# Performance work log

Measured on AMD Instinct MI355X. Metric: run time of the kernel, lower is better.

## Reference

```python
import jax, jax.numpy as jnp
import numpy as np
import math

D_MODEL = 1024
RANK = 128
K_RANK = 128
N_KNOW = 32768
COARSE_K = 64
FINE_K = 16
B, S = 2, 2048


def setup_inputs() -> dict:
    key = jax.random.key(0)
    ks = jax.random.split(key, 6)
    x = jax.random.normal(ks[0], (B, S, D_MODEL), dtype=jnp.float32)
    h = jax.random.normal(ks[1], (B, S, RANK), dtype=jnp.float32)
    W_router = jax.random.normal(ks[2], (D_MODEL, N_KNOW), dtype=jnp.float32) * 0.02
    W_q = jax.random.normal(ks[3], (K_RANK, RANK), dtype=jnp.float32) * 0.02  # Linear(rank->k_rank) weight
    K_all = jax.random.normal(ks[4], (N_KNOW, K_RANK), dtype=jnp.float32) * 0.02
    V_all = jax.random.normal(ks[5], (N_KNOW, D_MODEL), dtype=jnp.float32) * 0.02
    return {"x": x, "h": h, "W_router": W_router, "W_q": W_q, "K_all": K_all, "V_all": V_all}


def reference(x, h, W_router, W_q, K_all, V_all):
    # Stage 1: coarse candidate selection via router logits
    k_logits = jnp.einsum('bsd,dn->bsn', x, W_router)              # [B,S,N]
    coarse_scores, candidate_idx = jax.lax.top_k(k_logits, COARSE_K)  # [B,S,Ck]

    # Stage 2: fine matching with compressed query
    query = jnp.einsum('bsr,kr->bsk', h, W_q)                      # [B,S,K_RANK]
    K_cand = K_all[candidate_idx]                                  # [B,S,Ck,K_RANK] gather
    fine_scores = jnp.einsum('bsd,bscd->bsc', query, K_cand) / math.sqrt(K_RANK)
    fine_topk_scores, fine_local_idx = jax.lax.top_k(fine_scores, FINE_K)  # [B,S,Fk]
    fine_weights = jax.nn.softmax(fine_topk_scores, axis=-1)
    fine_global_idx = jnp.take_along_axis(candidate_idx, fine_local_idx, axis=-1)  # [B,S,Fk]

    selected_V = V_all[fine_global_idx]                            # [B,S,Fk,D] gather
    output = jnp.einsum('bsfd,bsf->bsd', selected_V, fine_weights)  # weighted combine
    return output
```

## Files before the change

kernel.cpp:

```cpp
#include <hip/hip_runtime.h>
#include <cstdint>

#define D_MODEL 1024
#define RANK 128
#define K_RANK_ 128
#define N_KNOW 32768
#define COARSE_K 64
#define FINE_K 16
#define NTOK 4096
#define MSEL 96
#define DELTA 1.15e-3f
#define SC 4096
#define QSCALE 8192.0f
#define QINV (1.0f / 8192.0f)

using u32 = unsigned int;
using u64 = unsigned long long;
typedef _Float16 half8 __attribute__((ext_vector_type(8)));
typedef __attribute__((ext_vector_type(4))) float f32x4;

__device__ __forceinline__ u32 ordf(float v) {
    u32 u = __float_as_uint(v);
    return (u & 0x80000000u) ? ~u : (u | 0x80000000u);
}
__device__ __forceinline__ ushort f2h(float f) {
    union { _Float16 h; ushort u; } cv; cv.h = (_Float16)f; return cv.u;
}
__device__ __forceinline__ void gload16(const void* g, void* l) {
    __builtin_amdgcn_global_load_lds(
        (const __attribute__((address_space(1))) char*)g,
        (__attribute__((address_space(3))) char*)l, 16, 0, 0);
}

__global__ __launch_bounds__(256)
void kcvt_x(const float* __restrict__ in, ushort* __restrict__ xh)
{
    int i = blockIdx.x * 256 + threadIdx.x;
    float4 v = ((const float4*)in)[i];
    ((ushort4*)xh)[i] = make_ushort4(f2h(v.x), f2h(v.y), f2h(v.z), f2h(v.w));
}

__global__ __launch_bounds__(256)
void kcvt_wt(const float* __restrict__ W, ushort* __restrict__ out, int col0)
{
    __shared__ float tile[32][33];
    const int nb = blockIdx.x * 32;
    const int kb = blockIdx.y * 32;
    const int tx = threadIdx.x & 31, ty = threadIdx.x >> 5;
#pragma unroll
    for (int q = 0; q < 4; ++q)
        tile[ty + q * 8][tx] = W[(size_t)(kb + ty + q * 8) * N_KNOW + col0 + nb + tx];
    __syncthreads();
#pragma unroll
    for (int q = 0; q < 4; ++q) {
        float v = tile[tx][ty + q * 8];
        out[(size_t)(nb + ty + q * 8) * D_MODEL + kb + tx] = f2h(v);
    }
}

__global__ __launch_bounds__(512, 2)
void k1f8(const ushort* __restrict__ xh, const ushort* __restrict__ wt,
          ushort* __restrict__ L)
{
    __shared__ ushort lds[2][32768];

    const int tid = threadIdx.x;
    const int nwg = gridDim.x;
    int wfl = blockIdx.x;
    wfl = (wfl & 7) * (nwg >> 3) + (wfl >> 3);
    const int bm = (wfl & 15) * 256;
    const int bn = (wfl >> 4) * 256;

    const int lane = tid & 63;
    const int wid = tid >> 6;
    const int wm = wid >> 2, wn = wid & 3;
    const int lr = lane & 15, g = lane >> 4;

    const ushort* gA[4]; const ushort* gB[4];
#pragma unroll
    for (int i = 0; i < 4; ++i) {
        const int o = i * 512 + tid;
        const int row = o >> 3;
        const int gslot = (o & 7) ^ (row & 7);
        gA[i] = xh + (size_t)(bm + row) * D_MODEL + gslot * 8;
        gB[i] = wt + (size_t)(bn + row) * D_MODEL + gslot * 8;
    }

    int aoff[2][8], boff[2][4];
#pragma unroll
    for (int ks = 0; ks < 2; ++ks) {
#pragma unroll
        for (int mf = 0; mf < 8; ++mf) {
            int row = wm * 128 + mf * 16 + lr;
            aoff[ks][mf] = row * 128 + (((ks * 4 + g) ^ (row & 7)) << 4);
        }
#pragma unroll
        for (int nf = 0; nf < 4; ++nf) {
            int row = wn * 64 + nf * 16 + lr;
            boff[ks][nf] = 32768 + row * 128 + (((ks * 4 + g) ^ (row & 7)) << 4);
        }
    }

    f32x4 acc[8][4];
#pragma unroll
    for (int mf = 0; mf < 8; ++mf)
#pragma unroll
        for (int nf = 0; nf < 4; ++nf) acc[mf][nf] = (f32x4)(0.f);

#define SAH(b, t, h)                                                           \
    {                                                                          \
        gload16(gA[2*(h)]   + (t) * 64,                                        \
                (char*)&lds[(b)][0] + ((2*(h)) * 512 + tid) * 16);             \
        gload16(gA[2*(h)+1] + (t) * 64,                                        \
                (char*)&lds[(b)][0] + ((2*(h)+1) * 512 + tid) * 16);           \
    }
#define SBH(b, t, h)                                                           \
    {                                                                          \
        gload16(gB[2*(h)]   + (t) * 64,                                        \
                (char*)&lds[(b)][0] + 32768 + ((2*(h)) * 512 + tid) * 16);     \
        gload16(gB[2*(h)+1] + (t) * 64,                                        \
                (char*)&lds[(b)][0] + 32768 + ((2*(h)+1) * 512 + tid) * 16);   \
    }

#define LDA4(lb, ks, base)                                                     \
    a0 = *(const half8*)((lb) + aoff[ks][(base) + 0]);                         \
    a1 = *(const half8*)((lb) + aoff[ks][(base) + 1]);                         \
    a2 = *(const half8*)((lb) + aoff[ks][(base) + 2]);                         \
    a3 = *(const half8*)((lb) + aoff[ks][(base) + 3]);

#define LDB4(lb, ks, bb)                                                       \
    bb[0] = *(const half8*)((lb) + boff[ks][0]);                               \
    bb[1] = *(const half8*)((lb) + boff[ks][1]);                               \
    bb[2] = *(const half8*)((lb) + boff[ks][2]);                               \
    bb[3] = *(const half8*)((lb) + boff[ks][3]);

#define MFMA16(mbase, bb)                                                      \
    __builtin_amdgcn_s_setprio(1);                                             \
    _Pragma("unroll")                                                          \
    for (int nf = 0; nf < 4; ++nf) {                                           \
        acc[(mbase)+0][nf] = __builtin_amdgcn_mfma_f32_16x16x32_f16(           \
            a0, bb[nf], acc[(mbase)+0][nf], 0, 0, 0);                          \
        acc[(mbase)+1][nf] = __builtin_amdgcn_mfma_f32_16x16x32_f16(           \
            a1, bb[nf], acc[(mbase)+1][nf], 0, 0, 0);                          \
        acc[(mbase)+2][nf] = __builtin_amdgcn_mfma_f32_16x16x32_f16(           \
            a2, bb[nf], acc[(mbase)+2][nf], 0, 0, 0);                          \
        acc[(mbase)+3][nf] = __builtin_amdgcn_mfma_f32_16x16x32_f16(           \
            a3, bb[nf], acc[(mbase)+3][nf], 0, 0, 0);                          \
    }                                                                          \
    __builtin_amdgcn_s_setprio(0);

#define SBAR()                                                                 \
    __builtin_amdgcn_sched_barrier(0);                                         \
    __builtin_amdgcn_s_barrier();                                              \
    __builtin_amdgcn_sched_barrier(0);

    SBH(0, 0, 0); SBH(0, 0, 1);
    SAH(0, 0, 0); SAH(0, 0, 1);
    SBH(1, 1, 0); SBH(1, 1, 1);

    const char* lb0 = (const char*)&lds[0][0];
    const char* lb1 = (const char*)&lds[1][0];
    half8 b0q[4], b1q[4];

    for (int i = 0; i < 8; ++i) {
        const int t1 = 2 * i + 1;
        const int tn0 = 2 * i + 2, tn1 = 2 * i + 3;
        const bool st = tn0 < 16;
        half8 a0, a1, a2, a3;

        asm volatile("s_waitcnt vmcnt(4)" ::: "memory");
        SBAR();
        LDA4(lb0, 0, 0);
        LDB4(lb0, 0, b0q);
        SAH(1, t1, 0);
        MFMA16(0, b0q);
        LDA4(lb0, 1, 0);
        LDB4(lb0, 1, b1q);
        SAH(1, t1, 1);
        MFMA16(0, b1q);
        SBAR();
        LDA4(lb0, 0, 4);
        if (st) SBH(0, tn0, 0);
        MFMA16(4, b0q);
        LDA4(lb0, 1, 4);
        if (st) SBH(0, tn0, 1);
        MFMA16(4, b1q);
        if (i < 7) asm volatile("s_waitcnt vmcnt(4)" ::: "memory");
        else       asm volatile("s_waitcnt vmcnt(0)" ::: "memory");
        SBAR();
        LDA4(lb1, 0, 0);
        LDB4(lb1, 0, b0q);
        if (st) SAH(0, tn0, 0);
        MFMA16(0, b0q);
        LDA4(lb1, 1, 0);
        LDB4(lb1, 1, b1q);
        if (st) SAH(0, tn0, 1);
        MFMA16(0, b1q);
        SBAR();
        LDA4(lb1, 0, 4);
        if (st) SBH(1, tn1, 0);
        MFMA16(4, b0q);
        LDA4(lb1, 1, 4);
        if (st) SBH(1, tn1, 1);
        MFMA16(4, b1q);
    }
#undef SAH
#undef SBH
#undef LDA4
#undef LDB4
#undef MFMA16
#undef SBAR

    const int crow0 = bm + wm * 128 + g * 4;
    const int ccol  = bn + wn * 64 + lr;
#pragma unroll
    for (int mf = 0; mf < 8; ++mf)
#pragma unroll
        for (int nf = 0; nf < 4; ++nf)
#pragma unroll
            for (int r = 0; r < 4; ++r) {
                int q = __float2int_rn(acc[mf][nf][r] * QSCALE) + 32768;
                q = q < 0 ? 0 : (q > 65535 ? 65535 : q);
                L[(size_t)(crow0 + mf * 16 + r) * SC + ccol + nf * 16] = (ushort)q;
            }
}

template <int M>
__global__ __launch_bounds__(256)
void k2_topk(const ushort* __restrict__ L, u64* __restrict__ R,
             int col0, int stripe)
{
    const int tt = blockIdx.x;
    const int tid = threadIdx.x;

    __shared__ u64 buf[4224];
    __shared__ int scnt;
    __shared__ int sred[4];

    u64 key[16];
    const uint4* row8 = (const uint4*)(L + (size_t)tt * SC);
#pragma unroll
    for (int q = 0; q < 2; ++q) {
        uint4 v = row8[q * 256 + tid];
        const int c = col0 + (q * 256 + tid) * 8;
        u32 wv[4] = {v.x, v.y, v.z, v.w};
#pragma unroll
        for (int d = 0; d < 4; ++d) {
            key[q * 8 + d * 2]     = ((u64)(wv[d] & 0xFFFFu) << 32) | (u32)(N_KNOW - 1 - (c + d * 2));
            key[q * 8 + d * 2 + 1] = ((u64)(wv[d] >> 16) << 32)    | (u32)(N_KNOW - 2 - (c + d * 2));
        }
    }

    u64 tkey;
    if (stripe == 0) {
        u32 lo = 0, hi = 65536;
        for (int it = 0; it < 17; ++it) {
            if (hi - lo <= 1) break;
            u32 mid = lo + ((hi - lo) >> 1);
            int c = 0;
#pragma unroll
            for (int j = 0; j < 16; ++j) c += ((u32)(key[j] >> 32) > mid) ? 1 : 0;
#pragma unroll
            for (int o = 32; o; o >>= 1) c += __shfl_xor(c, o);
            if ((tid & 63) == 0) sred[tid >> 6] = c;
            __syncthreads();
            c = sred[0] + sred[1] + sred[2] + sred[3];
            __syncthreads();
            if (c >= M) { lo = mid; if (c <= 768) break; }
            else hi = mid;
        }
        tkey = ((u64)lo << 32) | 0xFFFFFFFFull;
        if (tid == 0) scnt = 0;
    } else {
        tkey = R[(size_t)tt * M + (M - 1)];
        if (tid < M) buf[tid] = R[(size_t)tt * M + tid];
        if (tid == 0) scnt = M;
    }
    __syncthreads();

#pragma unroll
    for (int j = 0; j < 16; ++j)
        if (key[j] > tkey) {
            int p = atomicAdd(&scnt, 1);
            if (p < 4224) buf[p] = key[j];
        }
    __syncthreads();

    const int n = min(scnt, 4224);
    for (int i = tid; i < n; i += 256) {
        u64 ki = buf[i];
        int r = 0;
        for (int j = 0; j < n; ++j) r += (buf[j] > ki) ? 1 : 0;
        if (r < M) R[(size_t)tt * M + r] = ki;
    }
}

__global__ __launch_bounds__(256)
void k2b_band(const u64* __restrict__ R96, u32* __restrict__ jobs,
              int* __restrict__ jobCount, u32* __restrict__ band)
{
    __shared__ float sv[4][MSEL];
    const int tid = threadIdx.x;
    const int w = tid >> 6, lane = tid & 63;
    const int tt = blockIdx.x * 4 + w;

    sv[w][lane] = ((int)(u32)(R96[(size_t)tt * MSEL + lane] >> 32) - 32768) * QINV;
    if (lane < MSEL - 64)
        sv[w][lane + 64] = ((int)(u32)(R96[(size_t)tt * MSEL + lane + 64] >> 32) - 32768) * QINV;
    __syncthreads();

    const float t = sv[w][COARSE_K - 1];
    int cg = 0, cl = 0;
    for (int j = lane; j < MSEL; j += 64) {
        cg += (sv[w][j] > t + DELTA) ? 1 : 0;
        cl += (sv[w][j] < t - DELTA) ? 1 : 0;
    }
#pragma unroll
    for (int o = 32; o; o >>= 1) { cg += __shfl_xor(cg, o); cl += __shfl_xor(cl, o); }

    int lo = cg, hi = MSEL - 1 - cl;
    if (lo > COARSE_K - 1) lo = COARSE_K - 1;
    if (hi < COARSE_K - 1) hi = COARSE_K - 1;

    u32 b;
    if (lo == COARSE_K - 1 && hi == COARSE_K - 1) {
        b = 0x80000000u | 63u | (63u << 8);
    } else {
        int nj = hi - lo + 1;
        int base = 0;
        if (lane == 0) base = atomicAdd(jobCount, nj);
        base = __shfl(base, 0);
        for (int k = lane; k < nj; k += 64)
            jobs[base + k] = ((u32)tt << 8) | (u32)(lo + k);
        b = (u32)lo | ((u32)hi << 8);
    }
    if (lane == 0) band[tt] = b;
}

__global__ __launch_bounds__(256)
void k2b_exec(const u32* __restrict__ jobs, const int* __restrict__ jobCount,
              const u64* __restrict__ R96, const float* __restrict__ x,
              const float* __restrict__ W, u64* __restrict__ nk)
{
    __shared__ float red[4];
    const int tid = threadIdx.x;
    const int n = *jobCount;
    for (int j = blockIdx.x; j < n; j += gridDim.x) {
        u32 jd = jobs[j];
        int tt = jd >> 8, idx = jd & 255;
        u64 key = R96[(size_t)tt * MSEL + idx];
        int col = (N_KNOW - 1) - (int)(u32)(key & 0xFFFFFFFFu);
        float p = 0.f;
#pragma unroll
        for (int q = 0; q < 4; ++q) {
            int k = tid + q * 256;
            p = fmaf(x[(size_t)tt * D_MODEL + k], W[(size_t)k * N_KNOW + col], p);
        }
#pragma unroll
        for (int o = 32; o; o >>= 1) p += __shfl_xor(p, o);
        if ((tid & 63) == 0) red[tid >> 6] = p;
        __syncthreads();
        if (tid == 0) {
            float e = red[0] + red[1] + red[2] + red[3];
            nk[(size_t)tt * MSEL + idx] = ((u64)ordf(e) << 32) | (key & 0xFFFFFFFFu);
        }
        __syncthreads();
    }
}

__global__ __launch_bounds__(128)
void k2b_final(const u64* __restrict__ R96, const u64* __restrict__ nk,
               const u32* __restrict__ band, u64* __restrict__ R64)
{
    const int tt = blockIdx.x;
    const int tid = threadIdx.x;
    __shared__ u64 keys[MSEL];
    __shared__ u64 nkk[MSEL];

    const u32 b = band[tt];
    if (tid < MSEL) keys[tid] = R96[(size_t)tt * MSEL + tid];
    const int lo = b & 0xFF, hi = (b >> 8) & 0xFF;
    const bool trivial = (b & 0x80000000u) != 0;
    if (!trivial && tid >= lo && tid <= hi && tid < MSEL)
        nkk[tid] = nk[(size_t)tt * MSEL + tid];
    __syncthreads();

    if (trivial) {
        if (tid < COARSE_K) R64[(size_t)tt * COARSE_K + tid] = keys[tid];
        return;
    }
    if (tid < lo) R64[(size_t)tt * COARSE_K + tid] = keys[tid];
    const int mwin = COARSE_K - lo;
    if (tid >= lo && tid <= hi) {
        u64 me = nkk[tid];
        int r = 0;
        for (int j = lo; j <= hi; ++j) r += (nkk[j] > me) ? 1 : 0;
        if (r < mwin) R64[(size_t)tt * COARSE_K + lo + r] = keys[tid];
    }
}

__device__ __forceinline__ void fma4(float4& a, float w, const float4& v) {
    a.x = fmaf(w, v.x, a.x); a.y = fmaf(w, v.y, a.y);
    a.z = fmaf(w, v.z, a.z); a.w = fmaf(w, v.w, a.w);
}

__global__ __launch_bounds__(256)
void k3f(const float* __restrict__ h, const float* __restrict__ Wq,
         const float* __restrict__ Kall, const u64* __restrict__ R,
         int* __restrict__ fidx, float* __restrict__ fw)
{
    __shared__ float hq[4][RANK];
    __shared__ float qv[4][K_RANK_];

    const int tid = threadIdx.x;
    const int w = tid >> 6, lane = tid & 63;
    const int tt = blockIdx.x * 4 + w;

    {
        float2 hv = *(const float2*)(h + (size_t)tt * RANK + lane * 2);
        hq[w][lane * 2] = hv.x;
        hq[w][lane * 2 + 1] = hv.y;
    }
    const u64 key = R[(size_t)tt * COARSE_K + lane];
    const int ci = (N_KNOW - 1) - (int)(u32)(key & 0xFFFFFFFFu);
    __syncthreads();

    {
        float s0 = 0.f, s1 = 0.f;
        const float4* w0 = (const float4*)(Wq + (size_t)(lane * 2) * RANK);
        const float4* w1 = (const float4*)(Wq + (size_t)(lane * 2 + 1) * RANK);
#pragma unroll
        for (int r4 = 0; r4 < RANK / 4; ++r4) {
            float4 a = w0[r4], b = w1[r4];
            const float* hh = &hq[w][r4 * 4];
            s0 = fmaf(a.x, hh[0], s0); s0 = fmaf(a.y, hh[1], s0);
            s0 = fmaf(a.z, hh[2], s0); s0 = fmaf(a.w, hh[3], s0);
            s1 = fmaf(b.x, hh[0], s1); s1 = fmaf(b.y, hh[1], s1);
            s1 = fmaf(b.z, hh[2], s1); s1 = fmaf(b.w, hh[3], s1);
        }
        qv[w][lane * 2] = s0;
        qv[w][lane * 2 + 1] = s1;
    }
    __syncthreads();

    float sc;
    {
        float s = 0.f;
        const float4* kr = (const float4*)(Kall + (size_t)ci * K_RANK_);
#pragma unroll
        for (int r4 = 0; r4 < K_RANK_ / 4; ++r4) {
            float4 a = kr[r4];
            const float* qq = &qv[w][r4 * 4];
            s = fmaf(a.x, qq[0], s); s = fmaf(a.y, qq[1], s);
            s = fmaf(a.z, qq[2], s); s = fmaf(a.w, qq[3], s);
        }
        sc = s * 0.08838834764831845f;
    }

    const u64 myk = ((u64)ordf(sc) << 32) | (u32)(63 - lane);
    int rnk = 0;
#pragma unroll
    for (int j = 0; j < 64; ++j) {
        u64 kj = __shfl(myk, j);
        rnk += (kj > myk) ? 1 : 0;
    }

    float smax = sc;
#pragma unroll
    for (int o = 32; o; o >>= 1) smax = fmaxf(smax, __shfl_xor(smax, o));
    float e = (rnk < FINE_K) ? expf(sc - smax) : 0.f;
    float esum = e;
#pragma unroll
    for (int o = 32; o; o >>= 1) esum += __shfl_xor(esum, o);
    if (rnk < FINE_K) {
        fidx[(size_t)tt * FINE_K + rnk] = ci;
        fw[(size_t)tt * FINE_K + rnk] = e / esum;
    }
}

__global__ __launch_bounds__(256)
void k3g(const int* __restrict__ fidx, const float* __restrict__ fw,
         const float* __restrict__ Vall, float* __restrict__ out)
{
    __shared__ int si[FINE_K];
    __shared__ float sw[FINE_K];
    const int tt = blockIdx.x;
    const int tid = threadIdx.x;
    if (tid < FINE_K) {
        si[tid] = fidx[(size_t)tt * FINE_K + tid];
        sw[tid] = fw[(size_t)tt * FINE_K + tid];
    }
    __syncthreads();

    float4 a = make_float4(0.f, 0.f, 0.f, 0.f);
#pragma unroll
    for (int f = 0; f < FINE_K; ++f) {
        const float4 v = *(const float4*)(Vall + (size_t)si[f] * D_MODEL + tid * 4);
        fma4(a, sw[f], v);
    }
    ((float4*)(out + (size_t)tt * D_MODEL))[tid] = a;
}

extern "C" void kernel_launch(void* const* d_in, const int* in_sizes, int n_in,
                              void* d_out, int out_size, void* d_ws, size_t ws_size,
                              hipStream_t stream)
{
    const float* x  = (const float*)d_in[0];
    const float* h  = (const float*)d_in[1];
    const float* Wr = (const float*)d_in[2];
    const float* Wq = (const float*)d_in[3];
    const float* Ka = (const float*)d_in[4];
    const float* Va = (const float*)d_in[5];
    float* out = (float*)d_out;

    const size_t fixed =
        (size_t)NTOK * D_MODEL * 2 +
        (size_t)NTOK * SC * 2 +
        (size_t)NTOK * MSEL * 8 * 2 +
        (size_t)NTOK * COARSE_K * 8 +
        (size_t)NTOK * MSEL * 4 +
        4096 +
        (size_t)NTOK * 4 +
        (size_t)NTOK * FINE_K * 8;

    int WCH = N_KNOW;
    while (WCH > SC && fixed + (size_t)WCH * D_MODEL * 2 > ws_size)
        WCH >>= 1;

    char* p = (char*)d_ws;
    ushort* wt   = (ushort*)p;  p += (size_t)WCH * D_MODEL * 2;
    ushort* xh   = (ushort*)p;  p += (size_t)NTOK * D_MODEL * 2;
    ushort* Lq   = (ushort*)p;  p += (size_t)NTOK * SC * 2;
    u64*    R96  = (u64*)p;     p += (size_t)NTOK * MSEL * 8;
    u64*    nk   = (u64*)p;     p += (size_t)NTOK * MSEL * 8;
    u64*    R64  = (u64*)p;     p += (size_t)NTOK * COARSE_K * 8;
    u32*    jobs = (u32*)p;     p += (size_t)NTOK * MSEL * 4;
    int*    jobCount = (int*)p; p += 4096;
    u32*    band = (u32*)p;     p += (size_t)NTOK * 4;
    int*    fidx = (int*)p;     p += (size_t)NTOK * FINE_K * 4;
    float*  fw   = (float*)p;   p += (size_t)NTOK * FINE_K * 4;

    hipMemsetAsync(jobCount, 0, 4, stream);

    kcvt_x<<<NTOK * D_MODEL / 4 / 256, 256, 0, stream>>>(x, xh);

    const int nstripe = N_KNOW / SC;
    const int spc = WCH / SC;
    for (int s = 0; s < nstripe; ++s) {
        if (s % spc == 0)
            kcvt_wt<<<dim3(WCH / 32, D_MODEL / 32), 256, 0, stream>>>(Wr, wt, s * SC);
        const ushort* wts = wt + (size_t)((s % spc) * SC) * D_MODEL;
        k1f8<<<(SC / 256) * (NTOK / 256), 512, 0, stream>>>(xh, wts, Lq);
        k2_topk<MSEL><<<NTOK, 256, 0, stream>>>(Lq, R96, s * SC, s);
    }

    k2b_band<<<NTOK / 4, 256, 0, stream>>>(R96, jobs, jobCount, band);
    k2b_exec<<<8192, 256, 0, stream>>>(jobs, jobCount, R96, x, Wr, nk);
    k2b_final<<<NTOK, 128, 0, stream>>>(R96, nk, band, R64);

    k3f<<<NTOK / 4, 256, 0, stream>>>(h, Wq, Ka, R64, fidx, fw);
    k3g<<<NTOK, 256, 0, stream>>>(fidx, fw, Va, out);
}
```

Before: 764.0 us.

## Use split-fp16 transposed router weights for contiguous band rescoring

When the workspace is large enough, the router weight is converted once into transposed fp16 hi and lo halves. The rescoring kernel then reads contiguous hi+lo rows per candidate column instead of strided fp32 column reads of W_router. This targets the uncoalesced gather cost in k2b_exec. In exchange the conversion kernel writes an extra 64MB, and hi+lo is slightly less precise than fp32.

Result: faster. 689.3 us (-9.8%).

```diff
diff --git a/kernel.cpp b/kernel.cpp
--- a/kernel.cpp
+++ b/kernel.cpp
@@ -26,6 +26,9 @@
 __device__ __forceinline__ ushort f2h(float f) {
     union { _Float16 h; ushort u; } cv; cv.h = (_Float16)f; return cv.u;
 }
+__device__ __forceinline__ float h2f(ushort u) {
+    union { ushort u; _Float16 h; } cv; cv.u = u; return (float)cv.h;
+}
 __device__ __forceinline__ void gload16(const void* g, void* l) {
     __builtin_amdgcn_global_load_lds(
         (const __attribute__((address_space(1))) char*)g,
@@ -55,6 +58,29 @@
     for (int q = 0; q < 4; ++q) {
         float v = tile[tx][ty + q * 8];
         out[(size_t)(nb + ty + q * 8) * D_MODEL + kb + tx] = f2h(v);
+    }
+}
+
+__global__ __launch_bounds__(256)
+void kcvt_wt2(const float* __restrict__ W, ushort* __restrict__ hi,
+              ushort* __restrict__ lo)
+{
+    __shared__ float tile[32][33];
+    const int nb = blockIdx.x * 32;
+    const int kb = blockIdx.y * 32;
+    const int tx = threadIdx.x & 31, ty = threadIdx.x >> 5;
+#pragma unroll
+    for (int q = 0; q < 4; ++q)
+        tile[ty + q * 8][tx] = W[(size_t)(kb + ty + q * 8) * N_KNOW + nb + tx];
+    __syncthreads();
+#pragma unroll
+    for (int q = 0; q < 4; ++q) {
+        float v = tile[tx][ty + q * 8];
+        ushort hh = f2h(v);
+        ushort ll = f2h(v - h2f(hh));
+        size_t o = (size_t)(nb + ty + q * 8) * D_MODEL + kb + tx;
+        hi[o] = hh;
+        lo[o] = ll;
     }
 }
 
@@ -368,6 +394,40 @@
     }
 }
 
+__global__ __launch_bounds__(256)
+void k2b_exec_c(const u32* __restrict__ jobs, const int* __restrict__ jobCount,
+                const u64* __restrict__ R96, const float* __restrict__ x,
+                const ushort* __restrict__ whi, const ushort* __restrict__ wlo,
+                u64* __restrict__ nk)
+{
+    __shared__ float red[4];
+    const int tid = threadIdx.x;
+    const int n = *jobCount;
+    for (int j = blockIdx.x; j < n; j += gridDim.x) {
+        u32 jd = jobs[j];
+        int tt = jd >> 8, idx = jd & 255;
+        u64 key = R96[(size_t)tt * MSEL + idx];
+        int col = (N_KNOW - 1) - (int)(u32)(key & 0xFFFFFFFFu);
+        float4 xv = ((const float4*)(x + (size_t)tt * D_MODEL))[tid];
+        ushort4 hv = ((const ushort4*)(whi + (size_t)col * D_MODEL))[tid];
+        ushort4 lv = ((const ushort4*)(wlo + (size_t)col * D_MODEL))[tid];
+        float p = 0.f;
+        p = fmaf(xv.x, h2f(hv.x) + h2f(lv.x), p);
+        p = fmaf(xv.y, h2f(hv.y) + h2f(lv.y), p);
+        p = fmaf(xv.z, h2f(hv.z) + h2f(lv.z), p);
+        p = fmaf(xv.w, h2f(hv.w) + h2f(lv.w), p);
+#pragma unroll
+        for (int o = 32; o; o >>= 1) p += __shfl_xor(p, o);
+        if ((tid & 63) == 0) red[tid >> 6] = p;
+        __syncthreads();
+        if (tid == 0) {
+            float e = red[0] + red[1] + red[2] + red[3];
+            nk[(size_t)tt * MSEL + idx] = ((u64)ordf(e) << 32) | (key & 0xFFFFFFFFu);
+        }
+        __syncthreads();
+    }
+}
+
 __global__ __launch_bounds__(128)
 void k2b_final(const u64* __restrict__ R96, const u64* __restrict__ nk,
                const u32* __restrict__ band, u64* __restrict__ R64)
@@ -523,12 +583,23 @@
         (size_t)NTOK * 4 +
         (size_t)NTOK * FINE_K * 8;
 
-    int WCH = N_KNOW;
-    while (WCH > SC && fixed + (size_t)WCH * D_MODEL * 2 > ws_size)
-        WCH >>= 1;
+    const size_t WFULL = (size_t)N_KNOW * D_MODEL * 2;
+    const bool pathA = fixed + 2 * WFULL <= ws_size;
 
     char* p = (char*)d_ws;
-    ushort* wt   = (ushort*)p;  p += (size_t)WCH * D_MODEL * 2;
+    ushort* wt   = (ushort*)p;
+    ushort* wlo  = nullptr;
+    int WCH;
+    if (pathA) {
+        WCH = N_KNOW;
+        p += WFULL;
+        wlo = (ushort*)p; p += WFULL;
+    } else {
+        WCH = N_KNOW;
+        while (WCH > SC && fixed + (size_t)WCH * D_MODEL * 2 > ws_size)
+            WCH >>= 1;
+        p += (size_t)WCH * D_MODEL * 2;
+    }
     ushort* xh   = (ushort*)p;  p += (size_t)NTOK * D_MODEL * 2;
     ushort* Lq   = (ushort*)p;  p += (size_t)NTOK * SC * 2;
     u64*    R96  = (u64*)p;     p += (size_t)NTOK * MSEL * 8;
@@ -545,17 +616,29 @@
     kcvt_x<<<NTOK * D_MODEL / 4 / 256, 256, 0, stream>>>(x, xh);
 
     const int nstripe = N_KNOW / SC;
-    const int spc = WCH / SC;
-    for (int s = 0; s < nstripe; ++s) {
-        if (s % spc == 0)
-            kcvt_wt<<<dim3(WCH / 32, D_MODEL / 32), 256, 0, stream>>>(Wr, wt, s * SC);
-        const ushort* wts = wt + (size_t)((s % spc) * SC) * D_MODEL;
-        k1f8<<<(SC / 256) * (NTOK / 256), 512, 0, stream>>>(xh, wts, Lq);
-        k2_topk<MSEL><<<NTOK, 256, 0, stream>>>(Lq, R96, s * SC, s);
+    if (pathA) {
+        kcvt_wt2<<<dim3(N_KNOW / 32, D_MODEL / 32), 256, 0, stream>>>(Wr, wt, wlo);
+        for (int s = 0; s < nstripe; ++s) {
+            const ushort* wts = wt + (size_t)(s * SC) * D_MODEL;
+            k1f8<<<(SC / 256) * (NTOK / 256), 512, 0, stream>>>(xh, wts, Lq);
+            k2_topk<MSEL><<<NTOK, 256, 0, stream>>>(Lq, R96, s * SC, s);
+        }
+    } else {
+        const int spc = WCH / SC;
+        for (int s = 0; s < nstripe; ++s) {
+            if (s % spc == 0)
+                kcvt_wt<<<dim3(WCH / 32, D_MODEL / 32), 256, 0, stream>>>(Wr, wt, s * SC);
+            const ushort* wts = wt + (size_t)((s % spc) * SC) * D_MODEL;
+            k1f8<<<(SC / 256) * (NTOK / 256), 512, 0, stream>>>(xh, wts, Lq);
+            k2_topk<MSEL><<<NTOK, 256, 0, stream>>>(Lq, R96, s * SC, s);
+        }
     }
 
     k2b_band<<<NTOK / 4, 256, 0, stream>>>(R96, jobs, jobCount, band);
-    k2b_exec<<<8192, 256, 0, stream>>>(jobs, jobCount, R96, x, Wr, nk);
+    if (pathA)
+        k2b_exec_c<<<8192, 256, 0, stream>>>(jobs, jobCount, R96, x, wt, wlo, nk);
+    else
+        k2b_exec<<<8192, 256, 0, stream>>>(jobs, jobCount, R96, x, Wr, nk);
     k2b_final<<<NTOK, 128, 0, stream>>>(R96, nk, band, R64);
 
     k3f<<<NTOK / 4, 256, 0, stream>>>(h, Wq, Ka, R64, fidx, fw);
```

## Convert router weights once into hi/lo fp16 split and select top-k over full logit rows

Applied to the files above, without the earlier changes.

Transposes W_router a single time into fp16 hi and lo halves with a wider, vectorized transpose kernel. The exact rescoring pass now reads contiguous hi+lo rows instead of strided fp32 columns. When workspace allows, the logit GEMM runs once over all 32768 columns and a new single-pass per-token selection kernel replaces the eight stripe launches. This trades a much larger workspace and a 128 MB logit buffer round trip for fewer launches and coalesced rescoring. The hi+lo sum is slightly less exact than the original fp32 weights.

Result: slower. 1.891 ms (+147.5%).

```diff
diff --git a/kernel.cpp b/kernel.cpp
--- a/kernel.cpp
+++ b/kernel.cpp
@@ -26,6 +26,9 @@
 __device__ __forceinline__ ushort f2h(float f) {
     union { _Float16 h; ushort u; } cv; cv.h = (_Float16)f; return cv.u;
 }
+__device__ __forceinline__ float h2f(ushort u) {
+    union { ushort u; _Float16 h; } cv; cv.u = u; return (float)cv.h;
+}
 __device__ __forceinline__ void gload16(const void* g, void* l) {
     __builtin_amdgcn_global_load_lds(
         (const __attribute__((address_space(1))) char*)g,
@@ -41,26 +44,51 @@
 }
 
 __global__ __launch_bounds__(256)
-void kcvt_wt(const float* __restrict__ W, ushort* __restrict__ out, int col0)
-{
-    __shared__ float tile[32][33];
-    const int nb = blockIdx.x * 32;
-    const int kb = blockIdx.y * 32;
-    const int tx = threadIdx.x & 31, ty = threadIdx.x >> 5;
-#pragma unroll
-    for (int q = 0; q < 4; ++q)
-        tile[ty + q * 8][tx] = W[(size_t)(kb + ty + q * 8) * N_KNOW + col0 + nb + tx];
-    __syncthreads();
-#pragma unroll
-    for (int q = 0; q < 4; ++q) {
-        float v = tile[tx][ty + q * 8];
-        out[(size_t)(nb + ty + q * 8) * D_MODEL + kb + tx] = f2h(v);
+void kcvt_wt2v(const float* __restrict__ W, ushort* __restrict__ hi,
+               ushort* __restrict__ lo)
+{
+    __shared__ float tile[128][68];
+    const int nb = blockIdx.x * 64;
+    const int kb = blockIdx.y * 128;
+    const int tid = threadIdx.x;
+
+    {
+        const int lr = tid >> 4;
+        const int lc = tid & 15;
+#pragma unroll
+        for (int it = 0; it < 8; ++it) {
+            int kl = it * 16 + lr;
+            float4 v = *(const float4*)(W + (size_t)(kb + kl) * N_KNOW + nb + lc * 4);
+            *(float4*)&tile[kl][lc * 4] = v;
+        }
+    }
+    __syncthreads();
+
+    const int nl = tid >> 2;
+    const int tx = tid & 3;
+    u32 hw[16], lw[16];
+#pragma unroll
+    for (int s = 0; s < 16; ++s) {
+        float v0 = tile[tx * 32 + 2 * s][nl];
+        float v1 = tile[tx * 32 + 2 * s + 1][nl];
+        ushort h0 = f2h(v0), h1 = f2h(v1);
+        ushort l0 = f2h(v0 - h2f(h0)), l1 = f2h(v1 - h2f(h1));
+        hw[s] = (u32)h0 | ((u32)h1 << 16);
+        lw[s] = (u32)l0 | ((u32)l1 << 16);
+    }
+    size_t o = (size_t)(nb + nl) * D_MODEL + kb + tx * 32;
+#pragma unroll
+    for (int s4 = 0; s4 < 4; ++s4) {
+        *(uint4*)(hi + o + s4 * 8) =
+            make_uint4(hw[s4 * 4], hw[s4 * 4 + 1], hw[s4 * 4 + 2], hw[s4 * 4 + 3]);
+        *(uint4*)(lo + o + s4 * 8) =
+            make_uint4(lw[s4 * 4], lw[s4 * 4 + 1], lw[s4 * 4 + 2], lw[s4 * 4 + 3]);
     }
 }
 
 __global__ __launch_bounds__(512, 2)
 void k1f8(const ushort* __restrict__ xh, const ushort* __restrict__ wt,
-          ushort* __restrict__ L)
+          ushort* __restrict__ L, int Lstride)
 {
     __shared__ ushort lds[2][32768];
 
@@ -221,8 +249,81 @@
             for (int r = 0; r < 4; ++r) {
                 int q = __float2int_rn(acc[mf][nf][r] * QSCALE) + 32768;
                 q = q < 0 ? 0 : (q > 65535 ? 65535 : q);
-                L[(size_t)(crow0 + mf * 16 + r) * SC + ccol + nf * 16] = (ushort)q;
+                L[(size_t)(crow0 + mf * 16 + r) * Lstride + ccol + nf * 16] = (ushort)q;
             }
+}
+
+__global__ __launch_bounds__(256)
+void k2_full(const ushort* __restrict__ L, u64* __restrict__ R)
+{
+    const int tt = blockIdx.x;
+    const int tid = threadIdx.x;
+
+    __shared__ u64 buf[4224];
+    __shared__ int scnt;
+    __shared__ int sred[4];
+
+    const uint4* row8 = (const uint4*)(L + (size_t)tt * N_KNOW);
+    u64 key[16];
+
+#define LOADCHUNK(c)                                                           \
+    _Pragma("unroll")                                                          \
+    for (int q = 0; q < 2; ++q) {                                              \
+        uint4 v = row8[(c) * 512 + q * 256 + tid];                             \
+        const int cc = (c) * 4096 + (q * 256 + tid) * 8;                       \
+        u32 wv[4] = {v.x, v.y, v.z, v.w};                                      \
+        _Pragma("unroll")                                                      \
+        for (int d = 0; d < 4; ++d) {                                          \
+            key[q * 8 + d * 2]     = ((u64)(wv[d] & 0xFFFFu) << 32) | (u32)(N_KNOW - 1 - (cc + d * 2)); \
+            key[q * 8 + d * 2 + 1] = ((u64)(wv[d] >> 16) << 32)    | (u32)(N_KNOW - 2 - (cc + d * 2)); \
+        }                                                                      \
+    }
+
+#define FILTERKEYS()                                                           \
+    _Pragma("unroll")                                                          \
+    for (int j = 0; j < 16; ++j)                                               \
+        if (key[j] > tkey) {                                                   \
+            int p = atomicAdd(&scnt, 1);                                       \
+            if (p < 4224) buf[p] = key[j];                                     \
+        }
+
+    LOADCHUNK(0);
+    u32 lo = 0, hi = 65536;
+    for (int it = 0; it < 17; ++it) {
+        if (hi - lo <= 1) break;
+        u32 mid = lo + ((hi - lo) >> 1);
+        int c = 0;
+#pragma unroll
+        for (int j = 0; j < 16; ++j) c += ((u32)(key[j] >> 32) > mid) ? 1 : 0;
+#pragma unroll
+        for (int o = 32; o; o >>= 1) c += __shfl_xor(c, o);
+        if ((tid & 63) == 0) sred[tid >> 6] = c;
+        __syncthreads();
+        c = sred[0] + sred[1] + sred[2] + sred[3];
+        __syncthreads();
+        if (c >= MSEL) { lo = mid; if (c <= 768) break; }
+        else hi = mid;
+    }
+    const u64 tkey = ((u64)lo << 32) | 0xFFFFFFFFull;
+    if (tid == 0) scnt = 0;
+    __syncthreads();
+
+    FILTERKEYS();
+    for (int c = 1; c < 8; ++c) {
+        LOADCHUNK(c);
+        FILTERKEYS();
+    }
+    __syncthreads();
+#undef LOADCHUNK
+#undef FILTERKEYS
+
+    const int n = min(scnt, 4224);
+    for (int i = tid; i < n; i += 256) {
+        u64 ki = buf[i];
+        int r = 0;
+        for (int j = 0; j < n; ++j) r += (buf[j] > ki) ? 1 : 0;
+        if (r < MSEL) R[(size_t)tt * MSEL + r] = ki;
+    }
 }
 
 template <int M>
@@ -338,9 +439,10 @@
 }
 
 __global__ __launch_bounds__(256)
-void k2b_exec(const u32* __restrict__ jobs, const int* __restrict__ jobCount,
-              const u64* __restrict__ R96, const float* __restrict__ x,
-              const float* __restrict__ W, u64* __restrict__ nk)
+void k2b_exec_c(const u32* __restrict__ jobs, const int* __restrict__ jobCount,
+                const u64* __restrict__ R96, const float* __restrict__ x,
+                const ushort* __restrict__ whi, const ushort* __restrict__ wlo,
+                u64* __restrict__ nk)
 {
     __shared__ float red[4];
     const int tid = threadIdx.x;
@@ -350,12 +452,14 @@
         int tt = jd >> 8, idx = jd & 255;
         u64 key = R96[(size_t)tt * MSEL + idx];
         int col = (N_KNOW - 1) - (int)(u32)(key & 0xFFFFFFFFu);
+        float4 xv = ((const float4*)(x + (size_t)tt * D_MODEL))[tid];
+        ushort4 hv = ((const ushort4*)(whi + (size_t)col * D_MODEL))[tid];
+        ushort4 lv = ((const ushort4*)(wlo + (size_t)col * D_MODEL))[tid];
         float p = 0.f;
-#pragma unroll
-        for (int q = 0; q < 4; ++q) {
-            int k = tid + q * 256;
-            p = fmaf(x[(size_t)tt * D_MODEL + k], W[(size_t)k * N_KNOW + col], p);
-        }
+        p = fmaf(xv.x, h2f(hv.x) + h2f(lv.x), p);
+        p = fmaf(xv.y, h2f(hv.y) + h2f(lv.y), p);
+        p = fmaf(xv.z, h2f(hv.z) + h2f(lv.z), p);
+        p = fmaf(xv.w, h2f(hv.w) + h2f(lv.w), p);
 #pragma unroll
         for (int o = 32; o; o >>= 1) p += __shfl_xor(p, o);
         if ((tid & 63) == 0) red[tid >> 6] = p;
@@ -513,24 +617,25 @@
     const float* Va = (const float*)d_in[5];
     float* out = (float*)d_out;
 
-    const size_t fixed =
-        (size_t)NTOK * D_MODEL * 2 +
-        (size_t)NTOK * SC * 2 +
+    const size_t WFULL = (size_t)N_KNOW * D_MODEL * 2;
+    const size_t misc =
         (size_t)NTOK * MSEL * 8 * 2 +
         (size_t)NTOK * COARSE_K * 8 +
         (size_t)NTOK * MSEL * 4 +
         4096 +
         (size_t)NTOK * 4 +
         (size_t)NTOK * FINE_K * 8;
-
-    int WCH = N_KNOW;
-    while (WCH > SC && fixed + (size_t)WCH * D_MODEL * 2 > ws_size)
-        WCH >>= 1;
+    const size_t XHB = (size_t)NTOK * D_MODEL * 2;
+
+    const size_t LFULL = (size_t)NTOK * N_KNOW * 2;
+    const bool fullL = 2 * WFULL + XHB + LFULL + misc <= ws_size;
+    const size_t LBYTES = fullL ? LFULL : (size_t)NTOK * SC * 2;
 
     char* p = (char*)d_ws;
-    ushort* wt   = (ushort*)p;  p += (size_t)WCH * D_MODEL * 2;
-    ushort* xh   = (ushort*)p;  p += (size_t)NTOK * D_MODEL * 2;
-    ushort* Lq   = (ushort*)p;  p += (size_t)NTOK * SC * 2;
+    ushort* wt   = (ushort*)p;  p += WFULL;
+    ushort* wlo  = (ushort*)p;  p += WFULL;
+    ushort* xh   = (ushort*)p;  p += XHB;
+    ushort* Lq   = (ushort*)p;  p += LBYTES;
     u64*    R96  = (u64*)p;     p += (size_t)NTOK * MSEL * 8;
     u64*    nk   = (u64*)p;     p += (size_t)NTOK * MSEL * 8;
     u64*    R64  = (u64*)p;     p += (size_t)NTOK * COARSE_K * 8;
@@ -543,19 +648,21 @@
     hipMemsetAsync(jobCount, 0, 4, stream);
 
     kcvt_x<<<NTOK * D_MODEL / 4 / 256, 256, 0, stream>>>(x, xh);
-
-    const int nstripe = N_KNOW / SC;
-    const int spc = WCH / SC;
-    for (int s = 0; s < nstripe; ++s) {
-        if (s % spc == 0)
-            kcvt_wt<<<dim3(WCH / 32, D_MODEL / 32), 256, 0, stream>>>(Wr, wt, s * SC);
-        const ushort* wts = wt + (size_t)((s % spc) * SC) * D_MODEL;
-        k1f8<<<(SC / 256) * (NTOK / 256), 512, 0, stream>>>(xh, wts, Lq);
-        k2_topk<MSEL><<<NTOK, 256, 0, stream>>>(Lq, R96, s * SC, s);
+    kcvt_wt2v<<<dim3(N_KNOW / 64, D_MODEL / 128), 256, 0, stream>>>(Wr, wt, wlo);
+
+    if (fullL) {
+        k1f8<<<(N_KNOW / 256) * (NTOK / 256), 512, 0, stream>>>(xh, wt, Lq, N_KNOW);
+        k2_full<<<NTOK, 256, 0, stream>>>(Lq, R96);
+    } else {
+        for (int s = 0; s < N_KNOW / SC; ++s) {
+            const ushort* wts = wt + (size_t)(s * SC) * D_MODEL;
+            k1f8<<<(SC / 256) * (NTOK / 256), 512, 0, stream>>>(xh, wts, Lq, SC);
+            k2_topk<MSEL><<<NTOK, 256, 0, stream>>>(Lq, R96, s * SC, s);
+        }
     }
 
     k2b_band<<<NTOK / 4, 256, 0, stream>>>(R96, jobs, jobCount, band);
-    k2b_exec<<<8192, 256, 0, stream>>>(jobs, jobCount, R96, x, Wr, nk);
+    k2b_exec_c<<<8192, 256, 0, stream>>>(jobs, jobCount, R96, x, wt, wlo, nk);
     k2b_final<<<NTOK, 128, 0, stream>>>(R96, nk, band, R64);
 
     k3f<<<NTOK / 4, 256, 0, stream>>>(h, Wq, Ka, R64, fidx, fw);
```
